# Performance work log

Hardware: AMD Instinct MI355X
Metric: run time of the kernel (lower is better)

## Reference

```python
import jax, jax.numpy as jnp
import numpy as np
import math

HEADS = 5
CHANNELS = 320
SPLIT = CHANNELS // 2  # 160
LN_EPS = 1e-5


def _axial_attention(q, k, v, heads):
    # q,k,v: [B, N, D] with D = heads * c
    B, N, D = q.shape
    c = D // heads
    q = q.reshape(B, N, heads, c).transpose(0, 2, 1, 3)  # b h n c
    k = k.reshape(B, N, heads, c).transpose(0, 2, 1, 3)
    v = v.reshape(B, N, heads, c).transpose(0, 2, 1, 3)
    scores = jnp.einsum('bhnc,bhmc->bhnm', q, k) / math.sqrt(c)
    probs = jax.nn.softmax(scores, axis=-1)
    out = jnp.einsum('bhnm,bhmc->bhnc', probs, v)
    return out.transpose(0, 2, 1, 3).reshape(B, N, D)


def _linear(x, w, b):
    # torch nn.Linear: y = x @ w.T + b ; w: [out, in]
    return jnp.einsum('bnd,od->bno', x, w) + b


def setup_inputs() -> dict:
    key = jax.random.key(0)
    ks = jax.random.split(key, 20)
    s = 0.02
    inp = {
        'x': jax.random.normal(ks[0], (2, CHANNELS, 256, 256), dtype=jnp.float32),
        'ln_w': jnp.ones((CHANNELS,), jnp.float32),
        'ln_b': jnp.zeros((CHANNELS,), jnp.float32),
        'conv_w': jax.random.normal(ks[1], (CHANNELS, CHANNELS), jnp.float32) * s,
        'conv_b': jnp.zeros((CHANNELS,), jnp.float32),
    }
    names = ['qh', 'kh', 'vh', 'qv', 'kv', 'vv']
    for i, nm in enumerate(names):
        inp['w_' + nm] = jax.random.normal(ks[2 + i], (SPLIT, SPLIT), jnp.float32) * s
        inp['b_' + nm] = jnp.zeros((SPLIT,), jnp.float32)
    return inp


def reference(x, ln_w, ln_b, conv_w, conv_b,
              w_qh, b_qh, w_kh, b_kh, w_vh, b_vh,
              w_qv, b_qv, w_kv, b_kv, w_vv, b_vv):
    B, C, H, W = x.shape
    # LayerNorm over channel dim (applied after b c h w -> b h w c permute)
    mu = jnp.mean(x, axis=1, keepdims=True)
    var = jnp.mean((x - mu) ** 2, axis=1, keepdims=True)
    xn = (x - mu) / jnp.sqrt(var + LN_EPS)
    xn = xn * ln_w[None, :, None, None] + ln_b[None, :, None, None]
    # 1x1 conv
    xc = jnp.einsum('bchw,oc->bohw', xn, conv_w) + conv_b[None, :, None, None]
    x_h, x_v = xc[:, :SPLIT], xc[:, SPLIT:]
    # horizontal strips: b d h w -> (b h) w d
    xh = x_h.transpose(0, 2, 3, 1).reshape(B * H, W, SPLIT)
    # vertical strips: b d h w -> (b w) h d
    xv = x_v.transpose(0, 3, 2, 1).reshape(B * W, H, SPLIT)
    ah = _axial_attention(_linear(xh, w_qh, b_qh), _linear(xh, w_kh, b_kh),
                          _linear(xh, w_vh, b_vh), HEADS)
    av = _axial_attention(_linear(xv, w_qv, b_qv), _linear(xv, w_kv, b_kv),
                          _linear(xv, w_vv, b_vv), HEADS)
    attn_h = ah.reshape(B, H, W, SPLIT).transpose(0, 3, 1, 2)  # b d h w
    attn_v = av.reshape(B, W, H, SPLIT).transpose(0, 3, 2, 1)  # b d h w
    return jnp.concatenate([attn_h, attn_v], axis=0)  # [2B, SPLIT, H, W]
```

## Files before the change

### kernel.cpp

```cpp
#include <hip/hip_runtime.h>
#include <hip/hip_bf16.h>

typedef __attribute__((ext_vector_type(8))) short short8;
typedef __attribute__((ext_vector_type(4))) short short4v;
typedef __attribute__((ext_vector_type(4))) float floatx4;
typedef __hip_bfloat16 bf16;

__device__ __forceinline__ short f2bs(float f) {
  bf16 h = __float2bfloat16(f);
  return __builtin_bit_cast(short, h);
}
__device__ __forceinline__ float s2f(short s) {
  unsigned u = ((unsigned)(unsigned short)s) << 16;
  return __builtin_bit_cast(float, u);
}

__global__ void k_t2(const float* __restrict__ conv_w, const float* __restrict__ conv_b,
                     const float* __restrict__ ln_b, float* __restrict__ t2) {
  int k = blockIdx.x, t = threadIdx.x;
  float s = 0.f;
  for (int c = t; c < 320; c += 64) s += conv_w[k * 320 + c] * ln_b[c];
  #pragma unroll
  for (int off = 32; off; off >>= 1) s += __shfl_down(s, off);
  if (t == 0) t2[k] = s + conv_b[k];
}

struct WcArgs {
  const float* conv_w;
  const float* ln_w;
  const float* t2;
  const float* pw[6];
  const float* pb[6];
  bf16* Wc;
  float* bc;
};

__global__ void k_wc(WcArgs a) {
  int o = blockIdx.x, t = threadIdx.x;
  int branch = o >> 9, r = o & 511;
  bf16* wrow = a.Wc + (size_t)o * 320;
  if (r >= 480) {
    for (int c = t; c < 320; c += 64) wrow[c] = __float2bfloat16(0.f);
    if (t == 0) a.bc[o] = 0.f;
    return;
  }
  int qkv = r / 160, oc = r % 160;
  const float* pw = a.pw[branch * 3 + qkv];
  const float* pb = a.pb[branch * 3 + qkv];
  float scale = (qkv == 0) ? 0.17677669529663687f : 1.f;
  for (int c = t; c < 320; c += 64) {
    float acc = 0.f;
    for (int k = 0; k < 160; ++k)
      acc += pw[oc * 160 + k] * a.conv_w[(branch * 160 + k) * 320 + c];
    wrow[c] = __float2bfloat16(acc * a.ln_w[c] * scale);
  }
  float bacc = 0.f;
  for (int k = t; k < 160; k += 64) bacc += pw[oc * 160 + k] * a.t2[branch * 160 + k];
  #pragma unroll
  for (int off = 32; off; off >>= 1) bacc += __shfl_down(bacc, off);
  if (t == 0) a.bc[o] = (bacc + pb[oc]) * scale;
}

__global__ void k_xnt(const float* __restrict__ x, bf16* __restrict__ XnT, int b) {
  __shared__ float red[2][4][64];
  int t = threadIdx.x, w = t >> 6, l = t & 63;
  int pl = blockIdx.x * 64 + l;
  const float* xb = x + (size_t)b * 320 * 65536 + pl;
  float v[80];
  float sum = 0.f, ss = 0.f;
  #pragma unroll
  for (int i = 0; i < 80; ++i) {
    v[i] = xb[(size_t)(w * 80 + i) * 65536];
    sum += v[i]; ss += v[i] * v[i];
  }
  red[0][w][l] = sum; red[1][w][l] = ss;
  __syncthreads();
  float tsum = red[0][0][l] + red[0][1][l] + red[0][2][l] + red[0][3][l];
  float tss  = red[1][0][l] + red[1][1][l] + red[1][2][l] + red[1][3][l];
  float mean = tsum * (1.f / 320.f);
  float var = tss * (1.f / 320.f) - mean * mean;
  float rstd = rsqrtf(var + 1e-5f);
  float sh = -mean * rstd;
  short8* orow = (short8*)(XnT + (size_t)pl * 320 + w * 80);
  #pragma unroll
  for (int cc = 0; cc < 10; ++cc) {
    short8 o;
    #pragma unroll
    for (int j = 0; j < 8; ++j)
      o[j] = f2bs(fmaf(v[cc * 8 + j], rstd, sh));
    orow[cc] = o;
  }
}

__launch_bounds__(512)
__global__ void k_gemm(const bf16* __restrict__ Wc, const float* __restrict__ bc,
                       const bf16* __restrict__ XnT,
                       bf16* __restrict__ Yq, bf16* __restrict__ Yk, bf16* __restrict__ Yv) {
  __shared__ short As[256 * 40];
  __shared__ short Bs[128 * 40];
  int lin = blockIdx.x;
  int swz = (lin & 7) * 128 + (lin >> 3);
  int nb = swz >> 1, mb = swz & 1;
  int t = threadIdx.x, wv = t >> 6, l = t & 63;
  int wm = wv >> 1, wn = wv & 1;
  floatx4 acc[4][4];
  #pragma unroll
  for (int i = 0; i < 4; ++i)
    #pragma unroll
    for (int j = 0; j < 4; ++j) acc[i][j] = floatx4{0.f, 0.f, 0.f, 0.f};

  for (int k0 = 0; k0 < 320; k0 += 32) {
    __syncthreads();
    #pragma unroll
    for (int i = 0; i < 2; ++i) {
      int u = t + i * 512;
      int r = u >> 2, ch = u & 3;
      short8 v = *(const short8*)(Wc + (size_t)(mb * 256 + r) * 320 + k0 + ch * 8);
      *(short8*)(As + r * 40 + ch * 8) = v;
    }
    {
      int n = t >> 2, ch = t & 3;
      short8 v = *(const short8*)(XnT + (size_t)(nb * 128 + n) * 320 + k0 + ch * 8);
      *(short8*)(Bs + n * 40 + ch * 8) = v;
    }
    __syncthreads();
    short8 af[4], bfr[4];
    #pragma unroll
    for (int mt = 0; mt < 4; ++mt)
      af[mt] = *(const short8*)(As + (wm * 64 + mt * 16 + (l & 15)) * 40 + (l >> 4) * 8);
    #pragma unroll
    for (int nt = 0; nt < 4; ++nt)
      bfr[nt] = *(const short8*)(Bs + (wn * 64 + nt * 16 + (l & 15)) * 40 + (l >> 4) * 8);
    #pragma unroll
    for (int mt = 0; mt < 4; ++mt)
      #pragma unroll
      for (int nt = 0; nt < 4; ++nt)
        acc[mt][nt] = __builtin_amdgcn_mfma_f32_16x16x32_bf16(af[mt], bfr[nt], acc[mt][nt], 0, 0, 0);
  }

  #pragma unroll
  for (int mt = 0; mt < 4; ++mt) {
    int ob = mb * 256 + wm * 64 + mt * 16 + (l >> 4) * 4;
    if (ob >= 480) continue;
    int qkv = ob / 160, oc = ob % 160;
    bf16* yb = (qkv == 0) ? Yq : ((qkv == 1) ? Yk : Yv);
    floatx4 bias = *(const floatx4*)(bc + ob);
    #pragma unroll
    for (int nt = 0; nt < 4; ++nt) {
      int pl = nb * 128 + wn * 64 + nt * 16 + (l & 15);
      short4v o;
      #pragma unroll
      for (int r = 0; r < 4; ++r) o[r] = f2bs(acc[mt][nt][r] + bias[r]);
      *(short4v*)(yb + (size_t)pl * 160 + oc) = o;
    }
  }
}

__launch_bounds__(256, 2)
__global__ void k_attn(const bf16* __restrict__ Yq, const bf16* __restrict__ Yk,
                       const bf16* __restrict__ Yv, float* __restrict__ outF,
                       bf16* __restrict__ av, int vbranch) {
  __shared__ short Ks[256 * 40];
  __shared__ short Vt[32 * 264];
  __shared__ short Ps[64 * 264];
  __shared__ float rsum[64];
  int lin = blockIdx.x;
  int swz = (lin & 7) * 640 + (lin >> 3);
  int qb = swz & 3;
  int sh_ = swz >> 2;
  int s = sh_ & 255;
  int head = sh_ >> 8;
  int t = threadIdx.x, wv = t >> 6, l = t & 63;

  #pragma unroll
  for (int i = 0; i < 4; ++i) {
    int u = t + i * 256;
    int pos = u >> 2, ch = u & 3;
    size_t pix = vbranch ? ((size_t)pos * 256 + s) : ((size_t)s * 256 + pos);
    short8 kv = *(const short8*)(Yk + pix * 160 + head * 32 + ch * 8);
    *(short8*)(Ks + pos * 40 + ch * 8) = kv;
  }
  #pragma unroll
  for (int i = 0; i < 2; ++i) {
    int u = t + i * 256;
    int pp = u >> 2, ch = u & 3;
    int pos0 = pp * 2;
    size_t pix0 = vbranch ? ((size_t)pos0 * 256 + s) : ((size_t)s * 256 + pos0);
    size_t pix1 = vbranch ? ((size_t)(pos0 + 1) * 256 + s) : ((size_t)s * 256 + pos0 + 1);
    short8 v0 = *(const short8*)(Yv + pix0 * 160 + head * 32 + ch * 8);
    short8 v1 = *(const short8*)(Yv + pix1 * 160 + head * 32 + ch * 8);
    #pragma unroll
    for (int j = 0; j < 8; ++j) {
      unsigned pack = (unsigned)(unsigned short)v0[j] | ((unsigned)(unsigned short)v1[j] << 16);
      *(unsigned*)(Vt + (ch * 8 + j) * 264 + pos0) = pack;
    }
  }
  int qrow = qb * 64 + wv * 16 + (l & 15);
  size_t qpix = vbranch ? ((size_t)qrow * 256 + s) : ((size_t)s * 256 + qrow);
  short8 qf = *(const short8*)(Yq + qpix * 160 + head * 32 + (l >> 4) * 8);
  __syncthreads();

  float psum = 0.f;
  #pragma unroll
  for (int mt = 0; mt < 16; ++mt) {
    short8 kf = *(const short8*)(Ks + (mt * 16 + (l & 15)) * 40 + (l >> 4) * 8);
    floatx4 st = __builtin_amdgcn_mfma_f32_16x16x32_bf16(kf, qf, floatx4{0.f, 0.f, 0.f, 0.f}, 0, 0, 0);
    short4v pv;
    #pragma unroll
    for (int r = 0; r < 4; ++r) {
      float e = __expf(st[r]);
      psum += e;
      pv[r] = f2bs(e);
    }
    *(short4v*)(Ps + (wv * 16 + (l & 15)) * 264 + mt * 16 + (l >> 4) * 4) = pv;
  }
  psum += __shfl_xor(psum, 16);
  psum += __shfl_xor(psum, 32);
  if (l < 16) rsum[wv * 16 + l] = psum;
  __syncthreads();

  floatx4 oacc[2] = {floatx4{0.f, 0.f, 0.f, 0.f}, floatx4{0.f, 0.f, 0.f, 0.f}};
  #pragma unroll
  for (int kt = 0; kt < 8; ++kt) {
    short8 pf = *(const short8*)(Ps + (wv * 16 + (l & 15)) * 264 + kt * 32 + (l >> 4) * 8);
    #pragma unroll
    for (int nt = 0; nt < 2; ++nt) {
      short8 vf = *(const short8*)(Vt + (nt * 16 + (l & 15)) * 264 + kt * 32 + (l >> 4) * 8);
      oacc[nt] = __builtin_amdgcn_mfma_f32_16x16x32_bf16(pf, vf, oacc[nt], 0, 0, 0);
    }
  }
  floatx4 rs = *(const floatx4*)(rsum + wv * 16 + (l >> 4) * 4);
  #pragma unroll
  for (int nt = 0; nt < 2; ++nt) {
    int ch = head * 32 + nt * 16 + (l & 15);
    int p0 = qb * 64 + wv * 16 + (l >> 4) * 4;
    if (vbranch == 0) {
      floatx4 o;
      #pragma unroll
      for (int r = 0; r < 4; ++r) o[r] = oacc[nt][r] / rs[r];
      *(floatx4*)(outF + (size_t)ch * 65536 + s * 256 + p0) = o;
    } else {
      short4v o;
      #pragma unroll
      for (int r = 0; r < 4; ++r) o[r] = f2bs(oacc[nt][r] / rs[r]);
      *(short4v*)(av + (size_t)s * 40960 + ch * 256 + p0) = o;
    }
  }
}

__global__ void k_trans(const bf16* __restrict__ av, float* __restrict__ outb) {
  __shared__ short tile[64 * 68];
  int oc = blockIdx.x, w0 = blockIdx.y * 64, h0 = blockIdx.z * 64;
  int t = threadIdx.x;
  #pragma unroll
  for (int i = 0; i < 2; ++i) {
    int u = t + i * 256;
    int w_i = u >> 3, hc = u & 7;
    short8 v = *(const short8*)(av + (size_t)(w0 + w_i) * 40960 + oc * 256 + h0 + hc * 8);
    short4v lo = {v[0], v[1], v[2], v[3]}, hi = {v[4], v[5], v[6], v[7]};
    *(short4v*)(tile + w_i * 68 + hc * 8) = lo;
    *(short4v*)(tile + w_i * 68 + hc * 8 + 4) = hi;
  }
  __syncthreads();
  #pragma unroll
  for (int i = 0; i < 2; ++i) {
    int u = t + i * 256;
    int h_i = u >> 3, wc = u & 7;
    float* orow = outb + (size_t)oc * 65536 + (h0 + h_i) * 256 + w0 + wc * 8;
    floatx4 o0, o1;
    #pragma unroll
    for (int j = 0; j < 4; ++j) o0[j] = s2f(tile[(wc * 8 + j) * 68 + h_i]);
    #pragma unroll
    for (int j = 0; j < 4; ++j) o1[j] = s2f(tile[(wc * 8 + 4 + j) * 68 + h_i]);
    *(floatx4*)(orow) = o0;
    *(floatx4*)(orow + 4) = o1;
  }
}

extern "C" void kernel_launch(void* const* d_in, const int* in_sizes, int n_in,
                              void* d_out, int out_size, void* d_ws, size_t ws_size,
                              hipStream_t stream) {
  (void)in_sizes; (void)n_in; (void)out_size; (void)ws_size;
  const float* x      = (const float*)d_in[0];
  const float* ln_w   = (const float*)d_in[1];
  const float* ln_b   = (const float*)d_in[2];
  const float* conv_w = (const float*)d_in[3];
  const float* conv_b = (const float*)d_in[4];
  float* outF = (float*)d_out;

  char* ws = (char*)d_ws;
  bf16*  Wc  = (bf16*)ws;
  float* bc  = (float*)(ws + 655360);
  float* t2  = (float*)(ws + 659456);
  bf16*  XnT = (bf16*)(ws + 660736);
  bf16*  Y   = (bf16*)(ws + 660736 + 41943040ULL);
  bf16*  av  = (bf16*)(ws + 660736 + 41943040ULL + 62914560ULL);
  bf16* Yq = Y;
  bf16* Yk = Y + 10485760ULL;
  bf16* Yv = Y + 20971520ULL;

  k_t2<<<320, 64, 0, stream>>>(conv_w, conv_b, ln_b, t2);

  WcArgs wa;
  wa.conv_w = conv_w; wa.ln_w = ln_w; wa.t2 = t2; wa.Wc = Wc; wa.bc = bc;
  for (int br = 0; br < 2; ++br)
    for (int q = 0; q < 3; ++q) {
      wa.pw[br * 3 + q] = (const float*)d_in[5 + br * 6 + q * 2];
      wa.pb[br * 3 + q] = (const float*)d_in[6 + br * 6 + q * 2];
    }
  k_wc<<<1024, 64, 0, stream>>>(wa);

  for (int b = 0; b < 2; ++b) {
    k_xnt<<<1024, 256, 0, stream>>>(x, XnT, b);
    for (int branch = 0; branch < 2; ++branch) {
      k_gemm<<<1024, 512, 0, stream>>>(Wc + (size_t)branch * 512 * 320,
                                       bc + branch * 512, XnT, Yq, Yk, Yv);
      k_attn<<<5120, 256, 0, stream>>>(Yq, Yk, Yv,
                                       outF + (size_t)b * 160 * 65536, av, branch);
      if (branch == 1)
        k_trans<<<dim3(160, 4, 4), 256, 0, stream>>>(av, outF + (size_t)(2 + b) * 160 * 65536);
    }
  }
}
```

Measured before the change: 687.7 us.

## Merge both branches into single GEMM/attention launches and loop query blocks per CTA

```diff
diff --git a/kernel.cpp b/kernel.cpp
--- a/kernel.cpp
+++ b/kernel.cpp
@@ -94,13 +94,12 @@
 
 __launch_bounds__(512)
 __global__ void k_gemm(const bf16* __restrict__ Wc, const float* __restrict__ bc,
-                       const bf16* __restrict__ XnT,
-                       bf16* __restrict__ Yq, bf16* __restrict__ Yk, bf16* __restrict__ Yv) {
+                       const bf16* __restrict__ XnT, bf16* __restrict__ Yout) {
   __shared__ short As[256 * 40];
   __shared__ short Bs[128 * 40];
   int lin = blockIdx.x;
-  int swz = (lin & 7) * 128 + (lin >> 3);
-  int nb = swz >> 1, mb = swz & 1;
+  int swz = (lin & 7) * 256 + (lin >> 3);
+  int nb = swz >> 2, mb = swz & 3;
   int t = threadIdx.x, wv = t >> 6, l = t & 63;
   int wm = wv >> 1, wn = wv & 1;
   floatx4 acc[4][4];
@@ -141,9 +140,10 @@
   #pragma unroll
   for (int mt = 0; mt < 4; ++mt) {
     int ob = mb * 256 + wm * 64 + mt * 16 + (l >> 4) * 4;
-    if (ob >= 480) continue;
-    int qkv = ob / 160, oc = ob % 160;
-    bf16* yb = (qkv == 0) ? Yq : ((qkv == 1) ? Yk : Yv);
+    int br = ob >> 9, rr = ob & 511;
+    if (rr >= 480) continue;
+    int qkv = rr / 160, oc = rr % 160;
+    bf16* yb = Yout + (size_t)br * 31457280 + (size_t)qkv * 10485760;
     floatx4 bias = *(const floatx4*)(bc + ob);
     #pragma unroll
     for (int nt = 0; nt < 4; ++nt) {
@@ -157,26 +157,26 @@
 }
 
 __launch_bounds__(256, 2)
-__global__ void k_attn(const bf16* __restrict__ Yq, const bf16* __restrict__ Yk,
-                       const bf16* __restrict__ Yv, float* __restrict__ outF,
-                       bf16* __restrict__ av, int vbranch) {
+__global__ void k_attn(const bf16* __restrict__ Y, float* __restrict__ outF,
+                       bf16* __restrict__ av) {
   __shared__ short Ks[256 * 40];
   __shared__ short Vt[32 * 264];
   __shared__ short Ps[64 * 264];
   __shared__ float rsum[64];
   int lin = blockIdx.x;
-  int swz = (lin & 7) * 640 + (lin >> 3);
-  int qb = swz & 3;
-  int sh_ = swz >> 2;
-  int s = sh_ & 255;
-  int head = sh_ >> 8;
+  int vb = (lin >= 1280) ? 1 : 0;
+  int r2 = lin - vb * 1280;
+  int head = r2 >> 8, s = r2 & 255;
+  const bf16* Yq = Y + (size_t)vb * 31457280;
+  const bf16* Yk = Yq + 10485760;
+  const bf16* Yv = Yk + 10485760;
   int t = threadIdx.x, wv = t >> 6, l = t & 63;
 
   #pragma unroll
   for (int i = 0; i < 4; ++i) {
     int u = t + i * 256;
     int pos = u >> 2, ch = u & 3;
-    size_t pix = vbranch ? ((size_t)pos * 256 + s) : ((size_t)s * 256 + pos);
+    size_t pix = vb ? ((size_t)pos * 256 + s) : ((size_t)s * 256 + pos);
     short8 kv = *(const short8*)(Yk + pix * 160 + head * 32 + ch * 8);
     *(short8*)(Ks + pos * 40 + ch * 8) = kv;
   }
@@ -185,8 +185,8 @@
     int u = t + i * 256;
     int pp = u >> 2, ch = u & 3;
     int pos0 = pp * 2;
-    size_t pix0 = vbranch ? ((size_t)pos0 * 256 + s) : ((size_t)s * 256 + pos0);
-    size_t pix1 = vbranch ? ((size_t)(pos0 + 1) * 256 + s) : ((size_t)s * 256 + pos0 + 1);
+    size_t pix0 = vb ? ((size_t)pos0 * 256 + s) : ((size_t)s * 256 + pos0);
+    size_t pix1 = vb ? ((size_t)(pos0 + 1) * 256 + s) : ((size_t)s * 256 + pos0 + 1);
     short8 v0 = *(const short8*)(Yv + pix0 * 160 + head * 32 + ch * 8);
     short8 v1 = *(const short8*)(Yv + pix1 * 160 + head * 32 + ch * 8);
     #pragma unroll
@@ -195,56 +195,60 @@
       *(unsigned*)(Vt + (ch * 8 + j) * 264 + pos0) = pack;
     }
   }
-  int qrow = qb * 64 + wv * 16 + (l & 15);
-  size_t qpix = vbranch ? ((size_t)qrow * 256 + s) : ((size_t)s * 256 + qrow);
-  short8 qf = *(const short8*)(Yq + qpix * 160 + head * 32 + (l >> 4) * 8);
   __syncthreads();
 
-  float psum = 0.f;
-  #pragma unroll
-  for (int mt = 0; mt < 16; ++mt) {
-    short8 kf = *(const short8*)(Ks + (mt * 16 + (l & 15)) * 40 + (l >> 4) * 8);
-    floatx4 st = __builtin_amdgcn_mfma_f32_16x16x32_bf16(kf, qf, floatx4{0.f, 0.f, 0.f, 0.f}, 0, 0, 0);
-    short4v pv;
-    #pragma unroll
-    for (int r = 0; r < 4; ++r) {
-      float e = __expf(st[r]);
-      psum += e;
-      pv[r] = f2bs(e);
-    }
-    *(short4v*)(Ps + (wv * 16 + (l & 15)) * 264 + mt * 16 + (l >> 4) * 4) = pv;
-  }
-  psum += __shfl_xor(psum, 16);
-  psum += __shfl_xor(psum, 32);
-  if (l < 16) rsum[wv * 16 + l] = psum;
-  __syncthreads();
-
-  floatx4 oacc[2] = {floatx4{0.f, 0.f, 0.f, 0.f}, floatx4{0.f, 0.f, 0.f, 0.f}};
-  #pragma unroll
-  for (int kt = 0; kt < 8; ++kt) {
-    short8 pf = *(const short8*)(Ps + (wv * 16 + (l & 15)) * 264 + kt * 32 + (l >> 4) * 8);
+  for (int qb = 0; qb < 4; ++qb) {
+    int qrow = qb * 64 + wv * 16 + (l & 15);
+    size_t qpix = vb ? ((size_t)qrow * 256 + s) : ((size_t)s * 256 + qrow);
+    short8 qf = *(const short8*)(Yq + qpix * 160 + head * 32 + (l >> 4) * 8);
+
+    float psum = 0.f;
+    #pragma unroll
+    for (int mt = 0; mt < 16; ++mt) {
+      short8 kf = *(const short8*)(Ks + (mt * 16 + (l & 15)) * 40 + (l >> 4) * 8);
+      floatx4 st = __builtin_amdgcn_mfma_f32_16x16x32_bf16(kf, qf, floatx4{0.f, 0.f, 0.f, 0.f}, 0, 0, 0);
+      short4v pv;
+      #pragma unroll
+      for (int r = 0; r < 4; ++r) {
+        float e = __expf(st[r]);
+        psum += e;
+        pv[r] = f2bs(e);
+      }
+      *(short4v*)(Ps + (wv * 16 + (l & 15)) * 264 + mt * 16 + (l >> 4) * 4) = pv;
+    }
+    psum += __shfl_xor(psum, 16);
+    psum += __shfl_xor(psum, 32);
+    if (l < 16) rsum[wv * 16 + l] = psum;
+    __syncthreads();
+
+    floatx4 oacc[2] = {floatx4{0.f, 0.f, 0.f, 0.f}, floatx4{0.f, 0.f, 0.f, 0.f}};
+    #pragma unroll
+    for (int kt = 0; kt < 8; ++kt) {
+      short8 pf = *(const short8*)(Ps + (wv * 16 + (l & 15)) * 264 + kt * 32 + (l >> 4) * 8);
+      #pragma unroll
+      for (int nt = 0; nt < 2; ++nt) {
+        short8 vf = *(const short8*)(Vt + (nt * 16 + (l & 15)) * 264 + kt * 32 + (l >> 4) * 8);
+        oacc[nt] = __builtin_amdgcn_mfma_f32_16x16x32_bf16(pf, vf, oacc[nt], 0, 0, 0);
+      }
+    }
+    floatx4 rs = *(const floatx4*)(rsum + wv * 16 + (l >> 4) * 4);
     #pragma unroll
     for (int nt = 0; nt < 2; ++nt) {
-      short8 vf = *(const short8*)(Vt + (nt * 16 + (l & 15)) * 264 + kt * 32 + (l >> 4) * 8);
-      oacc[nt] = __builtin_amdgcn_mfma_f32_16x16x32_bf16(pf, vf, oacc[nt], 0, 0, 0);
-    }
-  }
-  floatx4 rs = *(const floatx4*)(rsum + wv * 16 + (l >> 4) * 4);
-  #pragma unroll
-  for (int nt = 0; nt < 2; ++nt) {
-    int ch = head * 32 + nt * 16 + (l & 15);
-    int p0 = qb * 64 + wv * 16 + (l >> 4) * 4;
-    if (vbranch == 0) {
-      floatx4 o;
-      #pragma unroll
-      for (int r = 0; r < 4; ++r) o[r] = oacc[nt][r] / rs[r];
-      *(floatx4*)(outF + (size_t)ch * 65536 + s * 256 + p0) = o;
-    } else {
-      short4v o;
-      #pragma unroll
-      for (int r = 0; r < 4; ++r) o[r] = f2bs(oacc[nt][r] / rs[r]);
-      *(short4v*)(av + (size_t)s * 40960 + ch * 256 + p0) = o;
-    }
+      int ch = head * 32 + nt * 16 + (l & 15);
+      int p0 = qb * 64 + wv * 16 + (l >> 4) * 4;
+      if (vb == 0) {
+        floatx4 o;
+        #pragma unroll
+        for (int r = 0; r < 4; ++r) o[r] = oacc[nt][r] / rs[r];
+        *(floatx4*)(outF + (size_t)ch * 65536 + s * 256 + p0) = o;
+      } else {
+        short4v o;
+        #pragma unroll
+        for (int r = 0; r < 4; ++r) o[r] = f2bs(oacc[nt][r] / rs[r]);
+        *(short4v*)(av + (size_t)s * 40960 + ch * 256 + p0) = o;
+      }
+    }
+    __syncthreads();
   }
 }
 
@@ -294,10 +298,7 @@
   float* t2  = (float*)(ws + 659456);
   bf16*  XnT = (bf16*)(ws + 660736);
   bf16*  Y   = (bf16*)(ws + 660736 + 41943040ULL);
-  bf16*  av  = (bf16*)(ws + 660736 + 41943040ULL + 62914560ULL);
-  bf16* Yq = Y;
-  bf16* Yk = Y + 10485760ULL;
-  bf16* Yv = Y + 20971520ULL;
+  bf16*  av  = (bf16*)(ws + 660736 + 41943040ULL + 125829120ULL);
 
   k_t2<<<320, 64, 0, stream>>>(conv_w, conv_b, ln_b, t2);
 
@@ -312,13 +313,8 @@
 
   for (int b = 0; b < 2; ++b) {
     k_xnt<<<1024, 256, 0, stream>>>(x, XnT, b);
-    for (int branch = 0; branch < 2; ++branch) {
-      k_gemm<<<1024, 512, 0, stream>>>(Wc + (size_t)branch * 512 * 320,
-                                       bc + branch * 512, XnT, Yq, Yk, Yv);
-      k_attn<<<5120, 256, 0, stream>>>(Yq, Yk, Yv,
-                                       outF + (size_t)b * 160 * 65536, av, branch);
-      if (branch == 1)
-        k_trans<<<dim3(160, 4, 4), 256, 0, stream>>>(av, outF + (size_t)(2 + b) * 160 * 65536);
-    }
-  }
-}
+    k_gemm<<<2048, 512, 0, stream>>>(Wc, bc, XnT, Y);
+    k_attn<<<2560, 256, 0, stream>>>(Y, outF + (size_t)b * 160 * 65536, av);
+    k_trans<<<dim3(160, 4, 4), 256, 0, stream>>>(av, outF + (size_t)(2 + b) * 160 * 65536);
+  }
+}
```

Result: faster. 658.9 us (-4.2%).
